# Kernel optimization log

Measured on AMD Instinct MI355X. Metric: run time of the kernel, lower is better.

Reference implementation:

```python
import jax, jax.numpy as jnp
import numpy as np

N = 50000      # nodes
E = 800000     # edges (avg degree 16)
F_IN = 128
H = 128
C = 64


def _lin(k, fan_in, fan_out):
    bound = 1.0 / np.sqrt(fan_in)
    kw, kb = jax.random.split(k)
    W = jax.random.uniform(kw, (fan_in, fan_out), jnp.float32, -bound, bound)
    b = jax.random.uniform(kb, (fan_out,), jnp.float32, -bound, bound)
    return W, b


def setup_inputs() -> dict:
    key = jax.random.key(0)
    ks = jax.random.split(key, 8)
    W1, b1 = _lin(ks[3], F_IN, H)
    W2, b2 = _lin(ks[4], H, H)
    W3, b3 = _lin(ks[5], H, H)
    Wr, br = _lin(ks[6], F_IN, H)
    Wo, bo = _lin(ks[7], H, C)
    return {
        "x": jax.random.normal(ks[0], (N, F_IN), jnp.float32),
        "src": jax.random.randint(ks[1], (E,), 0, N, jnp.int32),
        "dst": jax.random.randint(ks[2], (E,), 0, N, jnp.int32),
        "W1": W1, "b1": b1,
        "W2": W2, "b2": b2,
        "W3": W3, "b3": b3,
        "Wr": Wr, "br": br,
        "Wo": Wo, "bo": bo,
    }


def _degree_norms(src, dst, n):
    ones = jnp.ones(src.shape[0], jnp.float32)
    deg_out = jax.ops.segment_sum(ones, src, num_segments=n)
    deg_in = jax.ops.segment_sum(ones, dst, num_segments=n)
    # DGL norm='both': clamp zero-degree to 1 to avoid inf
    d_src = jnp.where(deg_out > 0, deg_out, 1.0) ** -0.5
    d_dst = jnp.where(deg_in > 0, deg_in, 1.0) ** -0.5
    return d_src, d_dst


def _graph_conv(x, W, b, src, dst, d_src, d_dst, n):
    # h = D_dst^{-1/2} A D_src^{-1/2} (x W) + b
    h = (x * d_src[:, None]) @ W              # [N, out]
    agg = jax.ops.segment_sum(h[src], dst, num_segments=n)  # SpMM via gather/scatter
    return agg * d_dst[:, None] + b


def reference(x, src, dst, W1, b1, W2, b2, W3, b3, Wr, br, Wo, bo):
    n = x.shape[0]
    d_src, d_dst = _degree_norms(src, dst, n)
    res = x @ Wr + br
    out = jax.nn.relu(_graph_conv(x, W1, b1, src, dst, d_src, d_dst, n))
    out = jax.nn.relu(_graph_conv(out, W2, b2, src, dst, d_src, d_dst, n))
    out = _graph_conv(out, W3, b3, src, dst, d_src, d_dst, n)
    out = jax.nn.relu(out + res)
    return out @ Wo + bo
```

## Files before the change

### kernel.cpp

```cpp
#include <hip/hip_runtime.h>
#include <cstdint>
#include <cstddef>

#define FD 128
#define CO 64
#define NB 256
#define NBINS 256

typedef short bf16x8 __attribute__((ext_vector_type(8)));
typedef float f32x4 __attribute__((ext_vector_type(4)));
typedef unsigned int uint32;
typedef unsigned char uint8;

__device__ __forceinline__ unsigned short f2bf(float f) {
  unsigned u = __float_as_uint(f);
  unsigned r = u + 0x7fffu + ((u >> 16) & 1u);
  return (unsigned short)(r >> 16);
}
__device__ __forceinline__ float bf2f(unsigned short b) {
  return __uint_as_float((unsigned)b << 16);
}


__global__ __launch_bounds__(256) void k_hist(const int* __restrict__ src,
                                              const int* __restrict__ dst,
                                              int* __restrict__ histD,
                                              int* __restrict__ histS,
                                              int E, int chunk) {
  __shared__ int hd[NBINS], hs[NBINS];
  int tid = threadIdx.x, blk = blockIdx.x;
  hd[tid] = 0;
  hs[tid] = 0;
  __syncthreads();
  int beg = blk * chunk;
  int end = min(E, beg + chunk);
  for (int e = beg + tid; e < end; e += 256) {
    atomicAdd(&hd[dst[e] >> 8], 1);
    atomicAdd(&hs[src[e] >> 8], 1);
  }
  __syncthreads();
  histD[tid * NB + blk] = hd[tid];
  histS[tid * NB + blk] = hs[tid];
}


__global__ __launch_bounds__(256) void k_ssum(int* __restrict__ a,
                                              int* __restrict__ b,
                                              int* __restrict__ bsums) {
  const int* p = blockIdx.y ? b : a;
  __shared__ int red[256];
  int tid = threadIdx.x;
  red[tid] = p[blockIdx.x * 256 + tid];
  __syncthreads();
  for (int o = 128; o > 0; o >>= 1) {
    if (tid < o) red[tid] += red[tid + o];
    __syncthreads();
  }
  if (tid == 0) bsums[blockIdx.y * 256 + blockIdx.x] = red[0];
}

__global__ __launch_bounds__(256) void k_sscan(int* __restrict__ bsums) {
  __shared__ int s[256];
  int tid = threadIdx.x;
  for (int r = 0; r < 2; r++) {
    int v = bsums[r * 256 + tid];
    s[tid] = v;
    __syncthreads();
    for (int o = 1; o < 256; o <<= 1) {
      int t = (tid >= o) ? s[tid - o] : 0;
      __syncthreads();
      s[tid] += t;
      __syncthreads();
    }
    bsums[r * 256 + tid] = s[tid] - v;
    __syncthreads();
  }
}

__global__ __launch_bounds__(256) void k_sapply(int* __restrict__ a,
                                                int* __restrict__ b,
                                                const int* __restrict__ bsums) {
  int* p = blockIdx.y ? b : a;
  int boff = bsums[blockIdx.y * 256 + blockIdx.x];
  __shared__ int s[256];
  int tid = threadIdx.x;
  int i = blockIdx.x * 256 + tid;
  int v = p[i];
  s[tid] = v;
  __syncthreads();
  for (int o = 1; o < 256; o <<= 1) {
    int t = (tid >= o) ? s[tid - o] : 0;
    __syncthreads();
    s[tid] += t;
    __syncthreads();
  }
  p[i] = boff + s[tid] - v;
}

__global__ __launch_bounds__(256) void k_scatter(const int* __restrict__ src,
                                                 const int* __restrict__ dst,
                                                 const int* __restrict__ offD,
                                                 const int* __restrict__ offS,
                                                 uint32* __restrict__ pk,
                                                 uint8* __restrict__ srcS8,
                                                 int E, int chunk) {
  __shared__ int runD[NBINS], runS[NBINS];
  int tid = threadIdx.x, blk = blockIdx.x;
  runD[tid] = offD[tid * NB + blk];
  runS[tid] = offS[tid * NB + blk];
  __syncthreads();
  int beg = blk * chunk;
  int end = min(E, beg + chunk);
  for (int e = beg + tid; e < end; e += 256) {
    int s = src[e], d = dst[e];
    int p = atomicAdd(&runD[d >> 8], 1);
    pk[p] = ((uint32)s << 8) | (uint32)(d & 255);
    int q = atomicAdd(&runS[s >> 8], 1);
    srcS8[q] = (uint8)(s & 255);
  }
}

__global__ __launch_bounds__(256) void k_bucket_dst(const uint32* __restrict__ pk,
                                                    const int* __restrict__ offD,
                                                    int* __restrict__ esrc,
                                                    int* __restrict__ row_ptr,
                                                    float* __restrict__ d_dst,
                                                    int N, int E) {
  __shared__ int cnt[NBINS], run[NBINS];
  int tid = threadIdx.x, bin = blockIdx.x;
  int start = offD[bin * NB];
  int end = (bin == NBINS - 1) ? E : offD[(bin + 1) * NB];
  cnt[tid] = 0;
  __syncthreads();
  for (int p = start + tid; p < end; p += 256) atomicAdd(&cnt[pk[p] & 255], 1);
  __syncthreads();
  int v = cnt[tid];
  run[tid] = v;
  __syncthreads();
  for (int o = 1; o < 256; o <<= 1) {
    int t = (tid >= o) ? run[tid - o] : 0;
    __syncthreads();
    run[tid] += t;
    __syncthreads();
  }
  int excl = run[tid] - v;
  int node = bin * 256 + tid;
  if (node < N) {
    row_ptr[node] = start + excl;
    d_dst[node] = rsqrtf((float)(v > 0 ? v : 1));
  }
  __syncthreads();
  run[tid] = start + excl;
  __syncthreads();
  for (int p = start + tid; p < end; p += 256) {
    uint32 v2 = pk[p];
    int slot = atomicAdd(&run[v2 & 255], 1);
    esrc[slot] = (int)(v2 >> 8);
  }
  if (bin == 0 && tid == 0) row_ptr[N] = E;
}

__global__ __launch_bounds__(256) void k_bucket_src(const uint8* __restrict__ srcS8,
                                                    const int* __restrict__ offS,
                                                    float* __restrict__ d_src,
                                                    int N, int E) {
  __shared__ int cnt[NBINS];
  int tid = threadIdx.x, bin = blockIdx.x;
  int start = offS[bin * NB];
  int end = (bin == NBINS - 1) ? E : offS[(bin + 1) * NB];
  cnt[tid] = 0;
  __syncthreads();
  for (int p = start + tid; p < end; p += 256) atomicAdd(&cnt[srcS8[p]], 1);
  __syncthreads();
  int node = bin * 256 + tid;
  if (node < N) {
    int v = cnt[tid];
    d_src[node] = rsqrtf((float)(v > 0 ? v : 1));
  }
}


__global__ __launch_bounds__(256) void k_wsplit(const float* __restrict__ W1,
                                                const float* __restrict__ W2,
                                                const float* __restrict__ W3,
                                                const float* __restrict__ Wr,
                                                const float* __restrict__ Wo,
                                                bf16x8* __restrict__ Whg,
                                                bf16x8* __restrict__ Wlg) {
  int idx = blockIdx.x * 256 + threadIdx.x;
  if (idx >= 9216) return;
  int region = idx >> 11;
  if (idx >= 8192) region = 4;
  const float* W = (region == 0) ? W1 : (region == 1) ? W2 : (region == 2) ? W3
                   : (region == 3) ? Wr : Wo;
  int cols = (region < 4) ? FD : CO;
  int local = idx - region * 2048;
  int kc = local / cols, col = local - kc * cols;
  bf16x8 h, l;
#pragma unroll
  for (int j = 0; j < 8; j++) {
    float v = W[(size_t)(kc * 8 + j) * cols + col];
    unsigned short hb = f2bf(v);
    h[j] = (short)hb;
    l[j] = (short)f2bf(v - bf2f(hb));
  }
  Whg[idx] = h;
  Wlg[idx] = l;
}


template <int NCW, bool ABF16, bool SCALE, bool BIAS, bool OUTBF16>
__global__ __launch_bounds__(256) void k_gemm(const void* __restrict__ Av,
                                              const bf16x8* __restrict__ Wh,
                                              const bf16x8* __restrict__ Wl,
                                              const float* __restrict__ bias,
                                              const float* __restrict__ rscale,
                                              void* __restrict__ outv, int N) {
  constexpr int NF = NCW / 32;
  __shared__ bf16x8 Ah[1024];
  int tid = threadIdx.x;
  int rowBase = blockIdx.x * 64;

#pragma unroll
  for (int t = 0; t < 4; t++) {
    int p = t * 256 + tid;
    int kc = p >> 6, row = p & 63;
    int gr = rowBase + row;
    bf16x8 h = {0, 0, 0, 0, 0, 0, 0, 0};
    if (gr < N) {
      if (ABF16) {
        h = *(const bf16x8*)((const unsigned short*)Av + (size_t)gr * FD + kc * 8);
      } else {
        const float4* A4 = (const float4*)((const float*)Av + (size_t)gr * FD + kc * 8);
        float4 u = A4[0];
        float4 v = A4[1];
        float vals[8] = {u.x, u.y, u.z, u.w, v.x, v.y, v.z, v.w};
#pragma unroll
        for (int j = 0; j < 8; j++) h[j] = (short)f2bf(vals[j]);
      }
    }
    Ah[kc * 64 + row] = h;
  }
  __syncthreads();

  int wv = tid >> 6, lane = tid & 63;
  int wr = (wv >> 1) * 32;
  int wc = (wv & 1) * (NCW / 2);
  int lhi = lane >> 4, llo = lane & 15;
  f32x4 acc[2][NF] = {};

#pragma unroll
  for (int ks = 0; ks < 4; ks++) {
    int kcg = ks * 4 + lhi;
    int abase = kcg * 64 + wr + llo;
    bf16x8 a0 = Ah[abase];
    bf16x8 a1 = Ah[abase + 16];
    int bbase = kcg * NCW + wc + llo;
#pragma unroll
    for (int nf = 0; nf < NF; nf++) {
      bf16x8 bh = Wh[bbase + nf * 16];
      bf16x8 bl = Wl[bbase + nf * 16];
      acc[0][nf] = __builtin_amdgcn_mfma_f32_16x16x32_bf16(a0, bh, acc[0][nf], 0, 0, 0);
      acc[1][nf] = __builtin_amdgcn_mfma_f32_16x16x32_bf16(a1, bh, acc[1][nf], 0, 0, 0);
      acc[0][nf] = __builtin_amdgcn_mfma_f32_16x16x32_bf16(a0, bl, acc[0][nf], 0, 0, 0);
      acc[1][nf] = __builtin_amdgcn_mfma_f32_16x16x32_bf16(a1, bl, acc[1][nf], 0, 0, 0);
    }
  }

  float rs[2][4];
  if (SCALE) {
#pragma unroll
    for (int mf = 0; mf < 2; mf++)
#pragma unroll
      for (int r = 0; r < 4; r++) {
        int row = rowBase + wr + mf * 16 + lhi * 4 + r;
        rs[mf][r] = (row < N) ? rscale[row] : 0.f;
      }
  }
#pragma unroll
  for (int nf = 0; nf < NF; nf++) {
    int col = wc + nf * 16 + llo;
    float bv = BIAS ? bias[col] : 0.f;
#pragma unroll
    for (int mf = 0; mf < 2; mf++) {
#pragma unroll
      for (int r = 0; r < 4; r++) {
        int row = rowBase + wr + mf * 16 + lhi * 4 + r;
        if (row < N) {
          float v = acc[mf][nf][r];
          if (SCALE) v *= rs[mf][r];
          v += bv;
          if (OUTBF16)
            ((unsigned short*)outv)[(size_t)row * NCW + col] = f2bf(v);
          else
            ((float*)outv)[(size_t)row * NCW + col] = v;
        }
      }
    }
  }
}


template <bool RELU, bool RES>
__global__ __launch_bounds__(256) void k_agg(const unsigned short* __restrict__ h,
                                             const int* __restrict__ row_ptr,
                                             const int* __restrict__ esrc,
                                             const float* __restrict__ d_dst,
                                             const float* __restrict__ bias,
                                             const unsigned short* __restrict__ res,
                                             unsigned short* __restrict__ out, int N) {
  int node = blockIdx.x * 4 + (threadIdx.x >> 6);
  int lane = threadIdx.x & 63;
  if (node >= N) return;
  int beg = row_ptr[node], end = row_ptr[node + 1];
  const uint32* h4 = (const uint32*)h;
  float ax = 0.f, ay = 0.f;
  int e = beg;
  for (; e + 4 <= end; e += 4) {
    int s0 = esrc[e + 0];
    int s1 = esrc[e + 1];
    int s2 = esrc[e + 2];
    int s3 = esrc[e + 3];
    uint32 v0 = h4[(size_t)s0 * 64 + lane];
    uint32 v1 = h4[(size_t)s1 * 64 + lane];
    uint32 v2 = h4[(size_t)s2 * 64 + lane];
    uint32 v3 = h4[(size_t)s3 * 64 + lane];
    ax += bf2f((unsigned short)(v0 & 0xffff)) + bf2f((unsigned short)(v1 & 0xffff)) +
          bf2f((unsigned short)(v2 & 0xffff)) + bf2f((unsigned short)(v3 & 0xffff));
    ay += bf2f((unsigned short)(v0 >> 16)) + bf2f((unsigned short)(v1 >> 16)) +
          bf2f((unsigned short)(v2 >> 16)) + bf2f((unsigned short)(v3 >> 16));
  }
  for (; e < end; e++) {
    int s = esrc[e];
    uint32 v = h4[(size_t)s * 64 + lane];
    ax += bf2f((unsigned short)(v & 0xffff));
    ay += bf2f((unsigned short)(v >> 16));
  }
  float d = d_dst[node];
  float2 b = ((const float2*)bias)[lane];
  float vx = ax * d + b.x;
  float vy = ay * d + b.y;
  if (RES) {
    uint32 r = ((const uint32*)res)[(size_t)node * 64 + lane];
    vx += bf2f((unsigned short)(r & 0xffff));
    vy += bf2f((unsigned short)(r >> 16));
  }
  if (RELU) {
    vx = fmaxf(vx, 0.f);
    vy = fmaxf(vy, 0.f);
  }
  uint32 o = (uint32)f2bf(vx) | ((uint32)f2bf(vy) << 16);
  ((uint32*)out)[(size_t)node * 64 + lane] = o;
}


extern "C" void kernel_launch(void* const* d_in, const int* in_sizes, int n_in,
                              void* d_out, int out_size, void* d_ws, size_t ws_size,
                              hipStream_t stream) {
  (void)n_in; (void)out_size; (void)ws_size;
  const float* x  = (const float*)d_in[0];
  const int*   src = (const int*)d_in[1];
  const int*   dst = (const int*)d_in[2];
  const float* W1 = (const float*)d_in[3];
  const float* b1 = (const float*)d_in[4];
  const float* W2 = (const float*)d_in[5];
  const float* b2 = (const float*)d_in[6];
  const float* W3 = (const float*)d_in[7];
  const float* b3 = (const float*)d_in[8];
  const float* Wr = (const float*)d_in[9];
  const float* br = (const float*)d_in[10];
  const float* Wo = (const float*)d_in[11];
  const float* bo = (const float*)d_in[12];
  float* out = (float*)d_out;

  const int N = in_sizes[0] / FD;
  const int E = in_sizes[1];

  char* ws = (char*)d_ws;
  size_t off = 0;
  auto alloc = [&](size_t bytes) -> void* {
    void* p = ws + off;
    off += (bytes + 255) & ~size_t(255);
    return p;
  };
  int* histD   = (int*)alloc((size_t)NBINS * NB * 4);
  int* histS   = (int*)alloc((size_t)NBINS * NB * 4);
  int* bsums   = (int*)alloc(2 * 256 * 4);
  uint32* pk   = (uint32*)alloc((size_t)E * 4);
  uint8* srcS8 = (uint8*)alloc((size_t)E);
  int* esrc    = (int*)alloc((size_t)E * 4);
  int* row_ptr = (int*)alloc((size_t)(N + 1) * 4);
  float* d_src = (float*)alloc((size_t)N * 4);
  float* d_dst = (float*)alloc((size_t)N * 4);
  bf16x8* Whg  = (bf16x8*)alloc(9216 * 16);
  bf16x8* Wlg  = (bf16x8*)alloc(9216 * 16);
  unsigned short* tb0  = (unsigned short*)alloc((size_t)N * FD * 2);
  unsigned short* tb1  = (unsigned short*)alloc((size_t)N * FD * 2);
  unsigned short* resb = (unsigned short*)alloc((size_t)N * FD * 2);

  int chunk = (E + NB - 1) / NB;
  dim3 gScan(256, 2);

  k_wsplit<<<36, 256, 0, stream>>>(W1, W2, W3, Wr, Wo, Whg, Wlg);
  k_hist<<<NB, 256, 0, stream>>>(src, dst, histD, histS, E, chunk);
  k_ssum<<<gScan, 256, 0, stream>>>(histD, histS, bsums);
  k_sscan<<<1, 256, 0, stream>>>(bsums);
  k_sapply<<<gScan, 256, 0, stream>>>(histD, histS, bsums);
  k_scatter<<<NB, 256, 0, stream>>>(src, dst, histD, histS, pk, srcS8, E, chunk);
  k_bucket_dst<<<NBINS, 256, 0, stream>>>(pk, histD, esrc, row_ptr, d_dst, N, E);
  k_bucket_src<<<NBINS, 256, 0, stream>>>(srcS8, histS, d_src, N, E);

  int gG = (N + 63) / 64;
  int gA = (N + 3) / 4;

  const bf16x8* Wh1 = Whg;
  const bf16x8* Wh2 = Whg + 2048;
  const bf16x8* Wh3 = Whg + 4096;
  const bf16x8* Whr = Whg + 6144;
  const bf16x8* Who = Whg + 8192;
  const bf16x8* Wl1 = Wlg;
  const bf16x8* Wl2 = Wlg + 2048;
  const bf16x8* Wl3 = Wlg + 4096;
  const bf16x8* Wlr = Wlg + 6144;
  const bf16x8* Wlo = Wlg + 8192;

  k_gemm<FD, false, false, true, true><<<gG, 256, 0, stream>>>(x, Whr, Wlr, br, nullptr, resb, N);
  k_gemm<FD, false, true, false, true><<<gG, 256, 0, stream>>>(x, Wh1, Wl1, nullptr, d_src, tb0, N);
  k_agg<true, false><<<gA, 256, 0, stream>>>(tb0, row_ptr, esrc, d_dst, b1, nullptr, tb1, N);
  k_gemm<FD, true, true, false, true><<<gG, 256, 0, stream>>>(tb1, Wh2, Wl2, nullptr, d_src, tb0, N);
  k_agg<true, false><<<gA, 256, 0, stream>>>(tb0, row_ptr, esrc, d_dst, b2, nullptr, tb1, N);
  k_gemm<FD, true, true, false, true><<<gG, 256, 0, stream>>>(tb1, Wh3, Wl3, nullptr, d_src, tb0, N);
  k_agg<true, true><<<gA, 256, 0, stream>>>(tb0, row_ptr, esrc, d_dst, b3, resb, tb1, N);
  k_gemm<CO, true, false, true, false><<<gG, 256, 0, stream>>>(tb1, Who, Wlo, bo, nullptr, out, N);
}
```

Measured before the change: 246.1 us.

## Fuse aggregation with following GEMM and merge first two x GEMMs

Merges the residual and first-layer GEMMs over x into one kernel that loads x once and runs two weight passes. Fuses each aggregation kernel with the next layer's GEMM: a block gathers 64 destination rows into XOR-swizzled LDS, applies bias, ReLU and the next layer's d_src scale, then multiplies by the next weights. This removes the intermediate bf16 round trips and several launches. In exchange, the grid for the gather phase drops from N/4 to N/64 blocks, and each wave now processes 16 nodes serially, which may reduce the memory parallelism available for the random gathers.

```diff
diff --git a/kernel.cpp b/kernel.cpp
--- a/kernel.cpp
+++ b/kernel.cpp
@@ -209,14 +209,16 @@
 }
 
 
-template <int NCW, bool ABF16, bool SCALE, bool BIAS, bool OUTBF16>
-__global__ __launch_bounds__(256) void k_gemm(const void* __restrict__ Av,
-                                              const bf16x8* __restrict__ Wh,
-                                              const bf16x8* __restrict__ Wl,
-                                              const float* __restrict__ bias,
-                                              const float* __restrict__ rscale,
-                                              void* __restrict__ outv, int N) {
-  constexpr int NF = NCW / 32;
+__global__ __launch_bounds__(256) void k_gemm_dual(const float* __restrict__ x,
+                                                   const bf16x8* __restrict__ Wh1,
+                                                   const bf16x8* __restrict__ Wl1,
+                                                   const float* __restrict__ d_src,
+                                                   const bf16x8* __restrict__ Whr,
+                                                   const bf16x8* __restrict__ Wlr,
+                                                   const float* __restrict__ br,
+                                                   unsigned short* __restrict__ out1,
+                                                   unsigned short* __restrict__ out2,
+                                                   int N) {
   __shared__ bf16x8 Ah[1024];
   int tid = threadIdx.x;
   int rowBase = blockIdx.x * 64;
@@ -228,22 +230,137 @@
     int gr = rowBase + row;
     bf16x8 h = {0, 0, 0, 0, 0, 0, 0, 0};
     if (gr < N) {
-      if (ABF16) {
-        h = *(const bf16x8*)((const unsigned short*)Av + (size_t)gr * FD + kc * 8);
-      } else {
-        const float4* A4 = (const float4*)((const float*)Av + (size_t)gr * FD + kc * 8);
-        float4 u = A4[0];
-        float4 v = A4[1];
-        float vals[8] = {u.x, u.y, u.z, u.w, v.x, v.y, v.z, v.w};
-#pragma unroll
-        for (int j = 0; j < 8; j++) h[j] = (short)f2bf(vals[j]);
-      }
+      const float4* A4 = (const float4*)(x + (size_t)gr * FD + kc * 8);
+      float4 u = A4[0];
+      float4 v = A4[1];
+      float vals[8] = {u.x, u.y, u.z, u.w, v.x, v.y, v.z, v.w};
+#pragma unroll
+      for (int j = 0; j < 8; j++) h[j] = (short)f2bf(vals[j]);
     }
     Ah[kc * 64 + row] = h;
   }
   __syncthreads();
 
   int wv = tid >> 6, lane = tid & 63;
+  int wr = (wv >> 1) * 32;
+  int wc = (wv & 1) * 64;
+  int lhi = lane >> 4, llo = lane & 15;
+
+#pragma unroll
+  for (int pass = 0; pass < 2; pass++) {
+    const bf16x8* Wh = pass ? Whr : Wh1;
+    const bf16x8* Wl = pass ? Wlr : Wl1;
+    f32x4 acc[2][4] = {};
+#pragma unroll
+    for (int ks = 0; ks < 4; ks++) {
+      int kcg = ks * 4 + lhi;
+      int abase = kcg * 64 + wr + llo;
+      bf16x8 a0 = Ah[abase];
+      bf16x8 a1 = Ah[abase + 16];
+      int bbase = kcg * FD + wc + llo;
+#pragma unroll
+      for (int nf = 0; nf < 4; nf++) {
+        bf16x8 bh = Wh[bbase + nf * 16];
+        bf16x8 bl = Wl[bbase + nf * 16];
+        acc[0][nf] = __builtin_amdgcn_mfma_f32_16x16x32_bf16(a0, bh, acc[0][nf], 0, 0, 0);
+        acc[1][nf] = __builtin_amdgcn_mfma_f32_16x16x32_bf16(a1, bh, acc[1][nf], 0, 0, 0);
+        acc[0][nf] = __builtin_amdgcn_mfma_f32_16x16x32_bf16(a0, bl, acc[0][nf], 0, 0, 0);
+        acc[1][nf] = __builtin_amdgcn_mfma_f32_16x16x32_bf16(a1, bl, acc[1][nf], 0, 0, 0);
+      }
+    }
+#pragma unroll
+    for (int nf = 0; nf < 4; nf++) {
+      int col = wc + nf * 16 + llo;
+      float bv = pass ? br[col] : 0.f;
+#pragma unroll
+      for (int mf = 0; mf < 2; mf++) {
+#pragma unroll
+        for (int r = 0; r < 4; r++) {
+          int row = rowBase + wr + mf * 16 + lhi * 4 + r;
+          if (row < N) {
+            float v = acc[mf][nf][r];
+            if (pass == 0) v *= d_src[row];
+            else v += bv;
+            unsigned short* o = pass ? out2 : out1;
+            o[(size_t)row * FD + col] = f2bf(v);
+          }
+        }
+      }
+    }
+  }
+}
+
+
+template <int NCW, bool RES, bool NEXTSCALE, bool BIASOUT, bool OUTBF16>
+__global__ __launch_bounds__(256) void k_aggemm(const unsigned short* __restrict__ h,
+                                                const int* __restrict__ row_ptr,
+                                                const int* __restrict__ esrc,
+                                                const float* __restrict__ d_dst,
+                                                const float* __restrict__ bias_in,
+                                                const float* __restrict__ d_src,
+                                                const unsigned short* __restrict__ res,
+                                                const bf16x8* __restrict__ Wh,
+                                                const bf16x8* __restrict__ Wl,
+                                                const float* __restrict__ bias_out,
+                                                void* __restrict__ outv, int N) {
+  constexpr int NF = NCW / 32;
+  __shared__ uint32 Alds[64 * 64];
+  int tid = threadIdx.x;
+  int wv = tid >> 6, lane = tid & 63;
+  int rowBase = blockIdx.x * 64;
+  const uint32* h4 = (const uint32*)h;
+  float2 bi = ((const float2*)bias_in)[lane];
+
+  for (int rr = 0; rr < 16; rr++) {
+    int r = wv * 16 + rr;
+    int gr = rowBase + r;
+    float vx = 0.f, vy = 0.f;
+    if (gr < N) {
+      int beg = row_ptr[gr], end = row_ptr[gr + 1];
+      float ax = 0.f, ay = 0.f;
+      int e = beg;
+      for (; e + 4 <= end; e += 4) {
+        int s0 = esrc[e + 0];
+        int s1 = esrc[e + 1];
+        int s2 = esrc[e + 2];
+        int s3 = esrc[e + 3];
+        uint32 v0 = h4[(size_t)s0 * 64 + lane];
+        uint32 v1 = h4[(size_t)s1 * 64 + lane];
+        uint32 v2 = h4[(size_t)s2 * 64 + lane];
+        uint32 v3 = h4[(size_t)s3 * 64 + lane];
+        ax += bf2f((unsigned short)(v0 & 0xffff)) + bf2f((unsigned short)(v1 & 0xffff)) +
+              bf2f((unsigned short)(v2 & 0xffff)) + bf2f((unsigned short)(v3 & 0xffff));
+        ay += bf2f((unsigned short)(v0 >> 16)) + bf2f((unsigned short)(v1 >> 16)) +
+              bf2f((unsigned short)(v2 >> 16)) + bf2f((unsigned short)(v3 >> 16));
+      }
+      for (; e < end; e++) {
+        int s = esrc[e];
+        uint32 v = h4[(size_t)s * 64 + lane];
+        ax += bf2f((unsigned short)(v & 0xffff));
+        ay += bf2f((unsigned short)(v >> 16));
+      }
+      float d = d_dst[gr];
+      vx = ax * d + bi.x;
+      vy = ay * d + bi.y;
+      if (RES) {
+        uint32 rv = ((const uint32*)res)[(size_t)gr * 64 + lane];
+        vx += bf2f((unsigned short)(rv & 0xffff));
+        vy += bf2f((unsigned short)(rv >> 16));
+      }
+      vx = fmaxf(vx, 0.f);
+      vy = fmaxf(vy, 0.f);
+      if (NEXTSCALE) {
+        float sc = d_src[gr];
+        vx *= sc;
+        vy *= sc;
+      }
+    }
+    uint32 o = (uint32)f2bf(vx) | ((uint32)f2bf(vy) << 16);
+    Alds[r * 64 + ((((lane >> 2) ^ (r & 7)) << 2) | (lane & 3))] = o;
+  }
+  __syncthreads();
+
+  const bf16x8* Ald8 = (const bf16x8*)Alds;
   int wr = (wv >> 1) * 32;
   int wc = (wv & 1) * (NCW / 2);
   int lhi = lane >> 4, llo = lane & 15;
@@ -252,9 +369,10 @@
 #pragma unroll
   for (int ks = 0; ks < 4; ks++) {
     int kcg = ks * 4 + lhi;
-    int abase = kcg * 64 + wr + llo;
-    bf16x8 a0 = Ah[abase];
-    bf16x8 a1 = Ah[abase + 16];
+    int row0 = wr + llo;
+    int row1 = wr + 16 + llo;
+    bf16x8 a0 = Ald8[row0 * 16 + (kcg ^ (row0 & 7))];
+    bf16x8 a1 = Ald8[row1 * 16 + (kcg ^ (row1 & 7))];
     int bbase = kcg * NCW + wc + llo;
 #pragma unroll
     for (int nf = 0; nf < NF; nf++) {
@@ -267,29 +385,17 @@
     }
   }
 
-  float rs[2][4];
-  if (SCALE) {
-#pragma unroll
-    for (int mf = 0; mf < 2; mf++)
-#pragma unroll
-      for (int r = 0; r < 4; r++) {
-        int row = rowBase + wr + mf * 16 + lhi * 4 + r;
-        rs[mf][r] = (row < N) ? rscale[row] : 0.f;
-      }
-  }
 #pragma unroll
   for (int nf = 0; nf < NF; nf++) {
     int col = wc + nf * 16 + llo;
-    float bv = BIAS ? bias[col] : 0.f;
+    float bv = BIASOUT ? bias_out[col] : 0.f;
 #pragma unroll
     for (int mf = 0; mf < 2; mf++) {
 #pragma unroll
       for (int r = 0; r < 4; r++) {
         int row = rowBase + wr + mf * 16 + lhi * 4 + r;
         if (row < N) {
-          float v = acc[mf][nf][r];
-          if (SCALE) v *= rs[mf][r];
-          v += bv;
+          float v = acc[mf][nf][r] + bv;
           if (OUTBF16)
             ((unsigned short*)outv)[(size_t)row * NCW + col] = f2bf(v);
           else
@@ -298,59 +404,6 @@
       }
     }
   }
-}
-
-
-template <bool RELU, bool RES>
-__global__ __launch_bounds__(256) void k_agg(const unsigned short* __restrict__ h,
-                                             const int* __restrict__ row_ptr,
-                                             const int* __restrict__ esrc,
-                                             const float* __restrict__ d_dst,
-                                             const float* __restrict__ bias,
-                                             const unsigned short* __restrict__ res,
-                                             unsigned short* __restrict__ out, int N) {
-  int node = blockIdx.x * 4 + (threadIdx.x >> 6);
-  int lane = threadIdx.x & 63;
-  if (node >= N) return;
-  int beg = row_ptr[node], end = row_ptr[node + 1];
-  const uint32* h4 = (const uint32*)h;
-  float ax = 0.f, ay = 0.f;
-  int e = beg;
-  for (; e + 4 <= end; e += 4) {
-    int s0 = esrc[e + 0];
-    int s1 = esrc[e + 1];
-    int s2 = esrc[e + 2];
-    int s3 = esrc[e + 3];
-    uint32 v0 = h4[(size_t)s0 * 64 + lane];
-    uint32 v1 = h4[(size_t)s1 * 64 + lane];
-    uint32 v2 = h4[(size_t)s2 * 64 + lane];
-    uint32 v3 = h4[(size_t)s3 * 64 + lane];
-    ax += bf2f((unsigned short)(v0 & 0xffff)) + bf2f((unsigned short)(v1 & 0xffff)) +
-          bf2f((unsigned short)(v2 & 0xffff)) + bf2f((unsigned short)(v3 & 0xffff));
-    ay += bf2f((unsigned short)(v0 >> 16)) + bf2f((unsigned short)(v1 >> 16)) +
-          bf2f((unsigned short)(v2 >> 16)) + bf2f((unsigned short)(v3 >> 16));
-  }
-  for (; e < end; e++) {
-    int s = esrc[e];
-    uint32 v = h4[(size_t)s * 64 + lane];
-    ax += bf2f((unsigned short)(v & 0xffff));
-    ay += bf2f((unsigned short)(v >> 16));
-  }
-  float d = d_dst[node];
-  float2 b = ((const float2*)bias)[lane];
-  float vx = ax * d + b.x;
-  float vy = ay * d + b.y;
-  if (RES) {
-    uint32 r = ((const uint32*)res)[(size_t)node * 64 + lane];
-    vx += bf2f((unsigned short)(r & 0xffff));
-    vy += bf2f((unsigned short)(r >> 16));
-  }
-  if (RELU) {
-    vx = fmaxf(vx, 0.f);
-    vy = fmaxf(vy, 0.f);
-  }
-  uint32 o = (uint32)f2bf(vx) | ((uint32)f2bf(vy) << 16);
-  ((uint32*)out)[(size_t)node * 64 + lane] = o;
 }
 
 
@@ -411,7 +464,6 @@
   k_bucket_src<<<NBINS, 256, 0, stream>>>(srcS8, histS, d_src, N, E);
 
   int gG = (N + 63) / 64;
-  int gA = (N + 3) / 4;
 
   const bf16x8* Wh1 = Whg;
   const bf16x8* Wh2 = Whg + 2048;
@@ -424,12 +476,11 @@
   const bf16x8* Wlr = Wlg + 6144;
   const bf16x8* Wlo = Wlg + 8192;
 
-  k_gemm<FD, false, false, true, true><<<gG, 256, 0, stream>>>(x, Whr, Wlr, br, nullptr, resb, N);
-  k_gemm<FD, false, true, false, true><<<gG, 256, 0, stream>>>(x, Wh1, Wl1, nullptr, d_src, tb0, N);
-  k_agg<true, false><<<gA, 256, 0, stream>>>(tb0, row_ptr, esrc, d_dst, b1, nullptr, tb1, N);
-  k_gemm<FD, true, true, false, true><<<gG, 256, 0, stream>>>(tb1, Wh2, Wl2, nullptr, d_src, tb0, N);
-  k_agg<true, false><<<gA, 256, 0, stream>>>(tb0, row_ptr, esrc, d_dst, b2, nullptr, tb1, N);
-  k_gemm<FD, true, true, false, true><<<gG, 256, 0, stream>>>(tb1, Wh3, Wl3, nullptr, d_src, tb0, N);
-  k_agg<true, true><<<gA, 256, 0, stream>>>(tb0, row_ptr, esrc, d_dst, b3, resb, tb1, N);
-  k_gemm<CO, true, false, true, false><<<gG, 256, 0, stream>>>(tb1, Who, Wlo, bo, nullptr, out, N);
-}
+  k_gemm_dual<<<gG, 256, 0, stream>>>(x, Wh1, Wl1, d_src, Whr, Wlr, br, tb0, resb, N);
+  k_aggemm<FD, false, true, false, true><<<gG, 256, 0, stream>>>(
+      tb0, row_ptr, esrc, d_dst, b1, d_src, nullptr, Wh2, Wl2, nullptr, tb1, N);
+  k_aggemm<FD, false, true, false, true><<<gG, 256, 0, stream>>>(
+      tb1, row_ptr, esrc, d_dst, b2, d_src, nullptr, Wh3, Wl3, nullptr, tb0, N);
+  k_aggemm<CO, true, false, true, false><<<gG, 256, 0, stream>>>(
+      tb0, row_ptr, esrc, d_dst, b3, nullptr, resb, Who, Wlo, bo, out, N);
+}
```

Result: slower. 310.5 us (+26.2%).
